# Performance work log

Hardware: AMD Instinct MI355X
Metric: run time of the kernel (lower is better)

## Reference

```python
import jax, jax.numpy as jnp
import numpy as np

N, G, HID, LAT, E_RAND = 20000, 3000, 256, 32, 320000
EPS = 1e-8
NEG_SLOPE = 0.2  # PyG GATv2Conv default leaky_relu slope


def _segment_softmax(logits, seg, n):
    # numerically stable softmax over edges grouped by destination node
    m = jax.ops.segment_max(logits, seg, num_segments=n)
    ex = jnp.exp(logits - m[seg])
    s = jax.ops.segment_sum(ex, seg, num_segments=n)
    return ex / (s[seg] + 1e-16)


def _gatv2(x, src, dst, Wl, Wr, att, b, n):
    # GATv2 (heads=1): score = att . leaky_relu(Wl x_j + Wr x_i)
    xl = x @ Wl  # [N, C] source transform (also the message)
    xr = x @ Wr  # [N, C] destination transform
    e = jax.nn.leaky_relu(xl[src] + xr[dst], NEG_SLOPE)  # [E, C]
    logit = e @ att  # [E]
    alpha = _segment_softmax(logit, dst, n)
    out = jax.ops.segment_sum(alpha[:, None] * xl[src], dst, num_segments=n)
    return out + b


def _log_zinb(x, mu, theta, pi):
    theta = theta[None, :]
    softplus_pi = jax.nn.softplus(-pi)
    log_theta_eps = jnp.log(theta + EPS)
    log_theta_mu_eps = jnp.log(theta + mu + EPS)
    pi_theta_log = -pi + theta * (log_theta_eps - log_theta_mu_eps)
    case_zero = jax.nn.softplus(pi_theta_log) - softplus_pi
    case_nz = (-softplus_pi + pi_theta_log
               + x * (jnp.log(mu + EPS) - log_theta_mu_eps)
               + jax.lax.lgamma(x + theta) - jax.lax.lgamma(theta)
               - jax.lax.lgamma(x + 1.0))
    return jnp.where(x < EPS, case_zero, 0.0) + jnp.where(x > EPS, case_nz, 0.0)


def setup_inputs():
    key = jax.random.key(0)
    ks = jax.random.split(key, 14)
    x = jax.random.randint(ks[0], (N, G), 0, 20).astype(jnp.float32)
    er = jax.random.randint(ks[1], (2, E_RAND), 0, N, dtype=jnp.int32)
    loops = jnp.tile(jnp.arange(N, dtype=jnp.int32)[None, :], (2, 1))
    edge_index = jnp.concatenate([er, loops], axis=1)  # [2, 340000] incl self-loops
    noise = jax.random.normal(ks[2], (N, LAT), dtype=jnp.float32)

    def init(k, shape, fan_in):
        return jax.random.normal(k, shape, dtype=jnp.float32) / np.float32(np.sqrt(fan_in))

    Wl1 = init(ks[3], (G, HID), G); Wr1 = init(ks[4], (G, HID), G)
    att1 = init(ks[5], (HID,), HID); b1 = jnp.zeros((HID,), jnp.float32)
    Wl2 = init(ks[6], (HID, 2 * LAT), HID); Wr2 = init(ks[7], (HID, 2 * LAT), HID)
    att2 = init(ks[8], (2 * LAT,), 2 * LAT); b2 = jnp.zeros((2 * LAT,), jnp.float32)
    Wd1 = init(ks[9], (LAT, HID), LAT); bd1 = jnp.zeros((HID,), jnp.float32)
    Wd2 = init(ks[10], (HID, G), HID); bd2 = jnp.zeros((G,), jnp.float32)
    Wdo = init(ks[11], (HID, G), HID); bdo = jnp.zeros((G,), jnp.float32)
    theta = jax.random.uniform(ks[12], (G,), minval=0.5, maxval=2.0, dtype=jnp.float32)
    return dict(x=x, edge_index=edge_index, noise=noise,
                Wl1=Wl1, Wr1=Wr1, att1=att1, b1=b1,
                Wl2=Wl2, Wr2=Wr2, att2=att2, b2=b2,
                Wd1=Wd1, bd1=bd1, Wd2=Wd2, bd2=bd2, Wdo=Wdo, bdo=bdo,
                theta=theta)


def reference(x, edge_index, noise, Wl1, Wr1, att1, b1, Wl2, Wr2, att2, b2,
              Wd1, bd1, Wd2, bd2, Wdo, bdo, theta):
    n = x.shape[0]
    src, dst = edge_index[0], edge_index[1]
    # --- GATv2 encoder ---
    h = _gatv2(x, src, dst, Wl1, Wr1, att1, b1, n)
    h2 = _gatv2(jax.nn.relu(h), src, dst, Wl2, Wr2, att2, b2, n)  # [N, 2*LAT]
    mu_z, logvar = h2[:, :LAT], h2[:, LAT:]
    # --- reparameterize: std = sqrt(exp(logvar)) ---
    z = mu_z + noise * jnp.exp(0.5 * logvar)
    # --- ZINB decoder ---
    hd = z @ Wd1 + bd1
    mean = jax.nn.softplus(hd @ Wd2 + bd2)
    pi = hd @ Wdo + bdo
    # --- loss: -E[log ZINB] + KL(q(z|x) || N(0,I)) ---
    recon = -jnp.mean(jnp.sum(_log_zinb(x, mean, theta, pi), axis=1))
    kl = jnp.mean(0.5 * jnp.sum(mu_z ** 2 + jnp.exp(logvar) - logvar - 1.0, axis=1))
    return recon + kl
```

## Files before the change

### kernel.cpp

```cpp
#include <hip/hip_runtime.h>
#include <math.h>

#define NN   20000
#define GG   3000
#define HIDD 256
#define LATT 32
#define KP1  3008
#define FEPS 1e-8f

typedef __attribute__((ext_vector_type(8))) __bf16 bf16x8;
typedef __attribute__((ext_vector_type(4))) float f32x4;

__device__ __forceinline__ float fsp(float v) {
    float t = __expf(-fabsf(v));
    return fmaxf(v, 0.f) + __logf(1.f + t);
}
__device__ __forceinline__ float sp_approx(float t) {
    float a = fabsf(t);
    float den = fmaf(a, fmaf(a, fmaf(a, 0.8382f, -1.4958f), 1.87f), 1.f);
    return fmaxf(t, 0.f) + 0.6931472f * __builtin_amdgcn_rcpf(den);
}
__device__ __forceinline__ float lrelu(float v) {
    return v > 0.f ? v : 0.2f * v;
}
__device__ __forceinline__ ushort f2bf(float f) {
    uint b = __float_as_uint(f);
    return (ushort)((b + 0x7FFFu + ((b >> 16) & 1u)) >> 16);
}
__device__ __forceinline__ float bf2f(ushort u) {
    return __uint_as_float((uint)u << 16);
}
__device__ __forceinline__ uint pk2(float a, float b) {
    return (uint)f2bf(a) | ((uint)f2bf(b) << 16);
}
__device__ __forceinline__ void gload16(const void* g, void* l) {
    __builtin_amdgcn_global_load_lds((const __attribute__((address_space(1))) void*)g,
                                     (__attribute__((address_space(3))) void*)l, 16, 0, 0);
}

__global__ __launch_bounds__(256)
void x2bf(const float* __restrict__ x, ushort* __restrict__ xb) {
    const int CH = KP1 / 8;
    size_t i = (size_t)blockIdx.x * 256 + threadIdx.x;
    if (i >= (size_t)NN * CH) return;
    size_t row = i / CH;
    int c8 = (int)(i % CH) * 8;
    uint4 w = make_uint4(0u, 0u, 0u, 0u);
    if (c8 < GG) {
        const float* p = x + row * GG + c8;
        float4 a = ((const float4*)p)[0];
        float4 b = ((const float4*)p)[1];
        w.x = pk2(a.x, a.y); w.y = pk2(a.z, a.w);
        w.z = pk2(b.x, b.y); w.w = pk2(b.z, b.w);
    }
    *(uint4*)(xb + row * KP1 + c8) = w;
}

__global__ void zinb_table(const float* __restrict__ theta, float* __restrict__ tabL,
                           float* __restrict__ logte, int G_) {
    int idx = blockIdx.x * blockDim.x + threadIdx.x;
    if (idx >= G_ * 20) return;
    int g = idx / 20, c = idx % 20;
    float th = theta[g];
    tabL[idx] = lgammaf((float)c + th) - lgammaf(th) - lgammaf((float)c + 1.f);
    if (c == 0) logte[g] = logf(th + FEPS);
}

__global__ void edge_hist(const int* __restrict__ ei, int* __restrict__ cnt, int E) {
    int e = blockIdx.x * blockDim.x + threadIdx.x;
    if (e < E) atomicAdd(&cnt[ei[E + e]], 1);
}

__global__ __launch_bounds__(1024)
void scan_deg(int* __restrict__ cnt_cur, int* __restrict__ rowptr, int Nn) {
    __shared__ int ts[1024];
    int t = threadIdx.x;
    int chunk = (Nn + 1023) / 1024;
    int beg = t * chunk, end = min(beg + chunk, Nn);
    int s = 0;
    for (int i = beg; i < end; i++) s += cnt_cur[i];
    ts[t] = s;
    __syncthreads();
    for (int off = 1; off < 1024; off <<= 1) {
        int v = (t >= off) ? ts[t - off] : 0;
        __syncthreads();
        ts[t] += v;
        __syncthreads();
    }
    int run = (t == 0) ? 0 : ts[t - 1];
    for (int i = beg; i < end; i++) {
        int c = cnt_cur[i];
        rowptr[i] = run;
        cnt_cur[i] = run;
        run += c;
    }
    if (t == 1023) rowptr[Nn] = ts[1023];
}

__global__ void edge_scatter(const int* __restrict__ ei, int* __restrict__ cur,
                             int* __restrict__ eidx, int E) {
    int e = blockIdx.x * blockDim.x + threadIdx.x;
    if (e < E) {
        int p = atomicAdd(&cur[ei[E + e]], 1);
        eidx[p] = e;
    }
}

__global__ __launch_bounds__(256)
void transp_bf16(const float* __restrict__ in, ushort* __restrict__ out,
                 int K, int N, int Kpad) {
    __shared__ ushort t[32][33];
    int k0 = blockIdx.x * 32, n0 = blockIdx.y * 32;
    int tx = threadIdx.x & 31, ty = threadIdx.x >> 5;
    #pragma unroll
    for (int u = 0; u < 32; u += 8) {
        int k = k0 + ty + u, n = n0 + tx;
        t[ty + u][tx] = (k < K && n < N) ? f2bf(in[(size_t)k * N + n]) : (ushort)0;
    }
    __syncthreads();
    #pragma unroll
    for (int u = 0; u < 32; u += 8) {
        int n = n0 + ty + u, k = k0 + tx;
        if (n < N && k < Kpad) out[(size_t)n * Kpad + k] = t[tx][ty + u];
    }
}

__global__ __launch_bounds__(256)
void wcomb(const float* __restrict__ Wd1, const float* __restrict__ bd1,
           const float* __restrict__ Wd2, const float* __restrict__ bd2,
           const float* __restrict__ Wdo, const float* __restrict__ bdo,
           ushort* __restrict__ W2t, ushort* __restrict__ Wot,
           float* __restrict__ b2c, float* __restrict__ boc, int G_) {
    __shared__ float w1s[32 * 256];
    int tid = threadIdx.x;
    for (int i = tid; i < 32 * 256; i += 256) w1s[i] = Wd1[i];
    __syncthreads();
    int gl = tid & 63, rg = tid >> 6;
    int g = blockIdx.x * 64 + gl;
    int gc = min(g, G_ - 1);
    float a2[8], ao[8];
    #pragma unroll
    for (int i = 0; i < 8; i++) { a2[i] = 0.f; ao[i] = 0.f; }
    float ab2 = 0.f, abo = 0.f;
    for (int j = 0; j < 256; j++) {
        float w2 = Wd2[(size_t)j * G_ + gc];
        float wo = Wdo[(size_t)j * G_ + gc];
        if (rg == 0) {
            float b1 = bd1[j];
            ab2 = fmaf(b1, w2, ab2);
            abo = fmaf(b1, wo, abo);
        }
        #pragma unroll
        for (int i = 0; i < 8; i++) {
            float w1 = w1s[(rg * 8 + i) * 256 + j];
            a2[i] = fmaf(w1, w2, a2[i]);
            ao[i] = fmaf(w1, wo, ao[i]);
        }
    }
    if (g < G_) {
        #pragma unroll
        for (int i = 0; i < 8; i++) {
            W2t[(size_t)g * 32 + rg * 8 + i] = f2bf(a2[i]);
            Wot[(size_t)g * 32 + rg * 8 + i] = f2bf(ao[i]);
        }
        if (rg == 0) { b2c[g] = ab2 + bd2[g]; boc[g] = abo + bdo[g]; }
    }
}

__global__ __launch_bounds__(256, 8)
void dec_zinb(const ushort* __restrict__ zb, const ushort* __restrict__ W2t,
              const ushort* __restrict__ Wot, const ushort* __restrict__ xb,
              const float* __restrict__ tabL, const float* __restrict__ theta,
              const float* __restrict__ logte, const float* __restrict__ b2c,
              const float* __restrict__ boc, double* __restrict__ partsR,
              int M, int G_) {
    __shared__ __align__(16) char xs[16384];
    __shared__ float tabs[64 * 20];
    __shared__ float thetas[64], thltes[64], bd2s[64], bdos[64];
    __shared__ double redd[4];
    const int tid = threadIdx.x;
    const int nwg = gridDim.x * gridDim.y;
    const int orig = blockIdx.y * gridDim.x + blockIdx.x;
    const int q = nwg >> 3, r = nwg & 7, xcd = orig & 7;
    const int vv = (xcd < r ? xcd * (q + 1) : r * (q + 1) + (xcd - r) * q) + (orig >> 3);
    const int bx = vv % gridDim.x, by = vv / gridDim.x;
    const int m0 = by * 128, n0 = bx * 64;
    const int lane = tid & 63, wid = tid >> 6;
    const int wr = wid >> 1, wc = wid & 1;
    const int frow = lane & 15;
    const int ksl = (lane >> 4) << 3;

    {
        const int row_in8 = lane >> 3;
        const int ch = lane & 7;
        #pragma unroll
        for (int u = 0; u < 4; u++) {
            int s = (wid << 2) + u;
            int rr = (s << 3) + row_in8;
            int gm = m0 + rr; if (gm > M - 1) gm = M - 1;
            int csw = ch ^ (rr & 7);
            size_t go = (size_t)gm * KP1 + n0 + (csw << 3);
            gload16(xb + go, xs + (s << 10) + (lane << 4));
        }
    }

    for (int i = tid; i < 64; i += 256) {
        int g = n0 + i;
        bool ok = g < G_;
        float th = ok ? theta[g] : 1.f;
        thetas[i] = th;
        thltes[i] = ok ? th * logte[g] : 0.f;
        bd2s[i]   = ok ? b2c[g] : 0.f;
        bdos[i]   = ok ? boc[g] : 0.f;
    }
    for (int i = tid; i < 64 * 20; i += 256) {
        int g = n0 + i / 20;
        tabs[i] = (g < G_) ? tabL[(size_t)g * 20 + i % 20] : 0.f;
    }

    f32x4 acc1[4][2], acc2[4][2];
    #pragma unroll
    for (int i = 0; i < 4; i++)
        #pragma unroll
        for (int j = 0; j < 2; j++) {
            acc1[i][j] = (f32x4){0.f, 0.f, 0.f, 0.f};
            acc2[i][j] = (f32x4){0.f, 0.f, 0.f, 0.f};
        }

    bf16x8 af[4];
    #pragma unroll
    for (int mi = 0; mi < 4; mi++) {
        int gm = min(m0 + (wr << 6) + (mi << 4) + frow, M - 1);
        af[mi] = *(const bf16x8*)(zb + (size_t)gm * 32 + ksl);
    }
    #pragma unroll
    for (int ni = 0; ni < 2; ni++) {
        int gn = min(n0 + (wc << 5) + (ni << 4) + frow, G_ - 1);
        bf16x8 bf1 = *(const bf16x8*)(W2t + (size_t)gn * 32 + ksl);
        bf16x8 bf2 = *(const bf16x8*)(Wot + (size_t)gn * 32 + ksl);
        #pragma unroll
        for (int mi = 0; mi < 4; mi++) {
            acc1[mi][ni] = __builtin_amdgcn_mfma_f32_16x16x32_bf16(af[mi], bf1, acc1[mi][ni], 0, 0, 0);
            acc2[mi][ni] = __builtin_amdgcn_mfma_f32_16x16x32_bf16(af[mi], bf2, acc2[mi][ni], 0, 0, 0);
        }
    }
    __syncthreads();

    const int lr = (lane >> 4) << 2;
    float lsum = 0.f;
    #pragma unroll
    for (int mi = 0; mi < 4; mi++)
        #pragma unroll
        for (int ni = 0; ni < 2; ni++) {
            int lcol = (wc << 5) + (ni << 4) + frow;
            int gn = n0 + lcol;
            int lrow0 = (wr << 6) + (mi << 4) + lr;
            if (gn >= G_) continue;
            f32x4 am = acc1[mi][ni], ap = acc2[mi][ni];
            float th = thetas[lcol], thlte = thltes[lcol];
            float bm = bd2s[lcol], bp = bdos[lcol];
            #pragma unroll
            for (int j = 0; j < 4; j++) {
                int lrow = lrow0 + j;
                if (m0 + lrow >= M) continue;
                int o = (lrow << 7) + ((((lcol >> 3) ^ (lrow & 7)) << 4)) + ((lcol & 7) << 1);
                float xv = bf2f(*(const ushort*)(xs + o));
                float mu  = fsp(am[j] + bm);
                float pi  = ap[j] + bp;
                float spp = fsp(pi);
                float ltme = __logf(th + mu + FEPS);
                float lmu  = __logf(mu + FEPS);
                int xi = (int)(xv + 0.5f);
                float ptl = fmaf(-th, ltme, thlte) - pi;
                float corr = (xv < FEPS) ? sp_approx(-ptl) : 0.f;
                lsum += thlte + tabs[lcol * 20 + xi] - spp
                      - (th + xv) * ltme + xv * lmu + corr;
            }
        }
    #pragma unroll
    for (int off = 32; off; off >>= 1) lsum += __shfl_down(lsum, off);
    if (lane == 0) redd[wid] = (double)lsum;
    __syncthreads();
    if (tid == 0)
        partsR[by * gridDim.x + bx] = redd[0] + redd[1] + redd[2] + redd[3];
}

__global__ __launch_bounds__(512, 4)
void gemm_big(const ushort* __restrict__ At, const ushort* __restrict__ B1t,
              const ushort* __restrict__ B2t, ushort* __restrict__ C1,
              ushort* __restrict__ C2, int M, int Kpad, int Nc) {
    __shared__ __align__(16) char lds[49152];
    char* ldsA  = lds;
    char* ldsB1 = lds + 16384;
    char* ldsB2 = lds + 32768;

    const int tid = threadIdx.x;
    const int nwg = gridDim.x * gridDim.y;
    const int orig = blockIdx.y * gridDim.x + blockIdx.x;
    const int q = nwg >> 3, r = nwg & 7, xcd = orig & 7;
    const int vv = (xcd < r ? xcd * (q + 1) : r * (q + 1) + (xcd - r) * q) + (orig >> 3);
    const int bx = vv % gridDim.x, by = vv / gridDim.x;
    const int m0 = by * 128, n0 = bx * 128;
    const int lane = tid & 63, wid = tid >> 6;
    const int wr = wid >> 2, wc = wid & 3;
    const int frow = lane & 15;
    const int fkb = (lane >> 4) << 4;

    const int row_in = lane >> 3;
    const int sch = (lane & 7) ^ (row_in & 7);
    const int ldso = (lane << 4);

    f32x4 acc1[4][2], acc2[4][2];
    #pragma unroll
    for (int i = 0; i < 4; i++)
        #pragma unroll
        for (int j = 0; j < 2; j++) {
            acc1[i][j] = (f32x4){0.f, 0.f, 0.f, 0.f};
            acc2[i][j] = (f32x4){0.f, 0.f, 0.f, 0.f};
        }

    const int nk = Kpad >> 6;
    for (int t = 0; t < nk; t++) {
        const int k0 = t << 6;
        #pragma unroll
        for (int u = 0; u < 2; u++) {
            int s = (wid << 1) + u;
            int gnb = n0 + (s << 3) + row_in;
            size_t gob = (size_t)gnb * Kpad + k0 + (sch << 3);
            gload16(B1t + gob, ldsB1 + (s << 10) + ldso);
            gload16(B2t + gob, ldsB2 + (s << 10) + ldso);
            int gma = m0 + (s << 3) + row_in;
            if (gma > M - 1) gma = M - 1;
            size_t goa = (size_t)gma * Kpad + k0 + (sch << 3);
            gload16(At + goa, ldsA + (s << 10) + ldso);
        }
        __syncthreads();
        #pragma unroll
        for (int kk = 0; kk < 2; kk++) {
            int kb = (kk << 6) + fkb;
            bf16x8 af[4], b1f[2], b2f[2];
            #pragma unroll
            for (int mi = 0; mi < 4; mi++) {
                int rr = (wr << 6) + (mi << 4) + frow;
                int o = ((rr << 7) + kb) ^ ((rr & 7) << 4);
                af[mi] = *(const bf16x8*)(ldsA + o);
            }
            #pragma unroll
            for (int ni = 0; ni < 2; ni++) {
                int rr = (wc << 5) + (ni << 4) + frow;
                int o = ((rr << 7) + kb) ^ ((rr & 7) << 4);
                b1f[ni] = *(const bf16x8*)(ldsB1 + o);
                b2f[ni] = *(const bf16x8*)(ldsB2 + o);
            }
            #pragma unroll
            for (int mi = 0; mi < 4; mi++)
                #pragma unroll
                for (int ni = 0; ni < 2; ni++) {
                    acc1[mi][ni] = __builtin_amdgcn_mfma_f32_16x16x32_bf16(af[mi], b1f[ni], acc1[mi][ni], 0, 0, 0);
                    acc2[mi][ni] = __builtin_amdgcn_mfma_f32_16x16x32_bf16(af[mi], b2f[ni], acc2[mi][ni], 0, 0, 0);
                }
        }
        __syncthreads();
    }

    const int lr = (lane >> 4) << 2;
    #pragma unroll
    for (int mi = 0; mi < 4; mi++)
        #pragma unroll
        for (int ni = 0; ni < 2; ni++) {
            int gmb = m0 + (wr << 6) + (mi << 4) + lr;
            int gn  = n0 + (wc << 5) + (ni << 4) + frow;
            if (gn >= Nc) continue;
            f32x4 v1 = acc1[mi][ni], v2 = acc2[mi][ni];
            #pragma unroll
            for (int j = 0; j < 4; j++) {
                int gm = gmb + j;
                if (gm < M) {
                    C1[(size_t)gm * Nc + gn] = f2bf(v1[j]);
                    C2[(size_t)gm * Nc + gn] = f2bf(v2[j]);
                }
            }
        }
}

__global__ __launch_bounds__(256, 4)
void mfma_dual(const void* __restrict__ Ap, const ushort* __restrict__ B1t,
               const ushort* __restrict__ B2t, float* __restrict__ C1,
               float* __restrict__ C2, int M, int K, int Nc) {
    __shared__ __align__(16) char lds[24576];
    char* ldsA  = lds;
    char* ldsB1 = lds + 8192;
    char* ldsB2 = lds + 16384;

    const int tid = threadIdx.x;
    const int m0 = blockIdx.y * 64, n0 = blockIdx.x * 64;
    const int lane = tid & 63, wid = tid >> 6;
    const int wr = wid >> 1, wc = wid & 1;
    const int frow = lane & 15;
    const int fkb = (lane >> 4) << 4;

    f32x4 acc1[2][2], acc2[2][2];
    #pragma unroll
    for (int i = 0; i < 2; i++)
        #pragma unroll
        for (int j = 0; j < 2; j++) {
            acc1[i][j] = (f32x4){0.f, 0.f, 0.f, 0.f};
            acc2[i][j] = (f32x4){0.f, 0.f, 0.f, 0.f};
        }

    const int nk = (K + 63) >> 6;
    for (int t = 0; t < nk; t++) {
        const int k0 = t << 6;
        #pragma unroll
        for (int u = 0; u < 2; u++) {
            int c = tid + (u << 8);
            int row = c >> 3, col8 = (c & 7) << 3;
            int gm = m0 + row, gk = k0 + col8;
            uint4 w = make_uint4(0u, 0u, 0u, 0u);
            if (gm < M && gk < K)
                w = *(const uint4*)((const ushort*)Ap + (size_t)gm * K + gk);
            int o = ((row << 7) + (col8 << 1)) ^ ((row & 7) << 4);
            *(uint4*)(ldsA + o) = w;
        }
        #pragma unroll
        for (int u = 0; u < 2; u++) {
            int c = tid + (u << 8);
            int row = c >> 3, col8 = (c & 7) << 3;
            int gn = n0 + row, gk = k0 + col8;
            uint4 w1 = make_uint4(0u, 0u, 0u, 0u), w2 = w1;
            if (gn < Nc && gk < K) {
                size_t o = (size_t)gn * K + gk;
                w1 = *(const uint4*)(B1t + o);
                w2 = *(const uint4*)(B2t + o);
            }
            int o = ((row << 7) + (col8 << 1)) ^ ((row & 7) << 4);
            *(uint4*)(ldsB1 + o) = w1;
            *(uint4*)(ldsB2 + o) = w2;
        }
        __syncthreads();
        #pragma unroll
        for (int kk = 0; kk < 2; kk++) {
            int kb = (kk << 6) + fkb;
            bf16x8 af[2], b1f[2], b2f[2];
            #pragma unroll
            for (int mi = 0; mi < 2; mi++) {
                int rr = (wr << 5) + (mi << 4) + frow;
                int o = ((rr << 7) + kb) ^ ((rr & 7) << 4);
                af[mi] = *(const bf16x8*)(ldsA + o);
            }
            #pragma unroll
            for (int ni = 0; ni < 2; ni++) {
                int rr = (wc << 5) + (ni << 4) + frow;
                int o = ((rr << 7) + kb) ^ ((rr & 7) << 4);
                b1f[ni] = *(const bf16x8*)(ldsB1 + o);
                b2f[ni] = *(const bf16x8*)(ldsB2 + o);
            }
            #pragma unroll
            for (int mi = 0; mi < 2; mi++)
                #pragma unroll
                for (int ni = 0; ni < 2; ni++) {
                    acc1[mi][ni] = __builtin_amdgcn_mfma_f32_16x16x32_bf16(af[mi], b1f[ni], acc1[mi][ni], 0, 0, 0);
                    acc2[mi][ni] = __builtin_amdgcn_mfma_f32_16x16x32_bf16(af[mi], b2f[ni], acc2[mi][ni], 0, 0, 0);
                }
        }
        __syncthreads();
    }

    const int lr = (lane >> 4) << 2;
    #pragma unroll
    for (int mi = 0; mi < 2; mi++)
        #pragma unroll
        for (int ni = 0; ni < 2; ni++) {
            int gmb = m0 + (wr << 5) + (mi << 4) + lr;
            int gn  = n0 + (wc << 5) + (ni << 4) + frow;
            if (gn >= Nc) continue;
            f32x4 v1 = acc1[mi][ni], v2 = acc2[mi][ni];
            #pragma unroll
            for (int j = 0; j < 4; j++) {
                int gm = gmb + j;
                if (gm < M) {
                    C1[(size_t)gm * Nc + gn] = v1[j];
                    C2[(size_t)gm * Nc + gn] = v2[j];
                }
            }
        }
}

template<int DW, int OM, int IBF>
__global__ __launch_bounds__(256)
void gat_attn(const void* __restrict__ xlv, const void* __restrict__ xrv,
              const float* __restrict__ att, const int* __restrict__ ei,
              const int* __restrict__ rowptr, const int* __restrict__ eidx,
              const float* __restrict__ bias, void* __restrict__ out,
              int D, int Nn) {
    int wid = threadIdx.x >> 6, lane = threadIdx.x & 63;
    int n = blockIdx.x * 4 + wid;
    if (n >= Nn) return;
    int k = lane * DW;
    float xrr[DW], ats[DW], hacc[DW];
    if (DW == 4) {
        float4 a4 = *(const float4*)(att + k);
        ats[0] = a4.x; ats[1] = a4.y; ats[2] = a4.z; ats[3] = a4.w;
        if (IBF) {
            ushort4 u = *(const ushort4*)((const ushort*)xrv + (size_t)n * D + k);
            xrr[0] = bf2f(u.x); xrr[1] = bf2f(u.y); xrr[2] = bf2f(u.z); xrr[3] = bf2f(u.w);
        } else {
            float4 r4 = *(const float4*)((const float*)xrv + (size_t)n * D + k);
            xrr[0] = r4.x; xrr[1] = r4.y; xrr[2] = r4.z; xrr[3] = r4.w;
        }
    } else {
        ats[0] = att[k];
        xrr[0] = IBF ? bf2f(((const ushort*)xrv)[(size_t)n * D + k])
                     : ((const float*)xrv)[(size_t)n * D + k];
    }
    #pragma unroll
    for (int d = 0; d < DW; d++) hacc[d] = 0.f;
    float m = -3.0e38f, ssum = 0.f;
    int beg = rowptr[n], end = rowptr[n + 1];
    for (int j = beg; j < end; j++) {
        int e = eidx[j];
        int src = ei[e];
        float v[DW];
        float p;
        if (DW == 4) {
            if (IBF) {
                ushort4 u = *(const ushort4*)((const ushort*)xlv + (size_t)src * D + k);
                v[0] = bf2f(u.x); v[1] = bf2f(u.y); v[2] = bf2f(u.z); v[3] = bf2f(u.w);
            } else {
                float4 v4 = *(const float4*)((const float*)xlv + (size_t)src * D + k);
                v[0] = v4.x; v[1] = v4.y; v[2] = v4.z; v[3] = v4.w;
            }
            p = ats[0] * lrelu(v[0] + xrr[0]) + ats[1] * lrelu(v[1] + xrr[1])
              + ats[2] * lrelu(v[2] + xrr[2]) + ats[3] * lrelu(v[3] + xrr[3]);
        } else {
            v[0] = IBF ? bf2f(((const ushort*)xlv)[(size_t)src * D + k])
                       : ((const float*)xlv)[(size_t)src * D + k];
            p = ats[0] * lrelu(v[0] + xrr[0]);
        }
        #pragma unroll
        for (int o2 = 32; o2; o2 >>= 1) p += __shfl_xor(p, o2);
        float mnew = fmaxf(m, p);
        float sc = __expf(m - mnew);
        float w  = __expf(p - mnew);
        ssum = fmaf(ssum, sc, w);
        #pragma unroll
        for (int d = 0; d < DW; d++) hacc[d] = fmaf(hacc[d], sc, w * v[d]);
        m = mnew;
    }
    float inv = 1.f / (ssum + 1e-16f);
    if (DW == 4) {
        float4 b = *(const float4*)(bias + k);
        float r0 = fmaf(hacc[0], inv, b.x), r1 = fmaf(hacc[1], inv, b.y);
        float r2 = fmaf(hacc[2], inv, b.z), r3 = fmaf(hacc[3], inv, b.w);
        if (OM == 0) {
            *(float4*)((float*)out + (size_t)n * D + k) = make_float4(r0, r1, r2, r3);
        } else {
            ushort4 o;
            o.x = f2bf(fmaxf(r0, 0.f)); o.y = f2bf(fmaxf(r1, 0.f));
            o.z = f2bf(fmaxf(r2, 0.f)); o.w = f2bf(fmaxf(r3, 0.f));
            *(ushort4*)((ushort*)out + (size_t)n * D + k) = o;
        }
    } else {
        float r0 = fmaf(hacc[0], inv, bias[k]);
        if (OM == 0) ((float*)out)[(size_t)n * D + k] = r0;
        else         ((ushort*)out)[(size_t)n * D + k] = f2bf(fmaxf(r0, 0.f));
    }
}

__global__ __launch_bounds__(256)
void z_kl(const float* __restrict__ h2, const float* __restrict__ noise,
          ushort* __restrict__ z, double* __restrict__ partsK, int Nn) {
    __shared__ double rd[4];
    int gid = blockIdx.x * blockDim.x + threadIdx.x;
    int n = gid >> 5, k = gid & 31;
    float kt = 0.f;
    if (n < Nn) {
        float mu = h2[(size_t)n * 64 + k];
        float lv = h2[(size_t)n * 64 + 32 + k];
        float ev = expf(lv);
        z[(size_t)n * 32 + k] = f2bf(mu + noise[(size_t)n * 32 + k] * expf(0.5f * lv));
        kt = 0.5f * (mu * mu + ev - lv - 1.f);
    }
    #pragma unroll
    for (int off = 32; off; off >>= 1) kt += __shfl_down(kt, off);
    int wid = threadIdx.x >> 6, lane = threadIdx.x & 63;
    if (lane == 0) rd[wid] = (double)kt;
    __syncthreads();
    if (threadIdx.x == 0) partsK[blockIdx.x] = rd[0] + rd[1] + rd[2] + rd[3];
}

__global__ __launch_bounds__(256)
void final_reduce(const double* __restrict__ pR, int nR,
                  const double* __restrict__ pK, int nK,
                  float* __restrict__ out, int Nn) {
    __shared__ double sd[256];
    double s = 0.0;
    for (int i = threadIdx.x; i < nR; i += 256) s -= pR[i];
    for (int i = threadIdx.x; i < nK; i += 256) s += pK[i];
    sd[threadIdx.x] = s;
    __syncthreads();
    for (int o = 128; o; o >>= 1) {
        if (threadIdx.x < o) sd[threadIdx.x] += sd[threadIdx.x + o];
        __syncthreads();
    }
    if (threadIdx.x == 0) out[0] = (float)(sd[0] / (double)Nn);
}

extern "C" void kernel_launch(void* const* d_in, const int* in_sizes, int n_in,
                              void* d_out, int out_size, void* d_ws, size_t ws_size,
                              hipStream_t stream) {
    const int N_ = NN, G_ = GG, HID_ = HIDD;
    const float* x     = (const float*)d_in[0];
    const int*   ei    = (const int*)d_in[1];
    const float* noise = (const float*)d_in[2];
    const float* Wl1   = (const float*)d_in[3];
    const float* Wr1   = (const float*)d_in[4];
    const float* att1  = (const float*)d_in[5];
    const float* b1    = (const float*)d_in[6];
    const float* Wl2   = (const float*)d_in[7];
    const float* Wr2   = (const float*)d_in[8];
    const float* att2  = (const float*)d_in[9];
    const float* b2    = (const float*)d_in[10];
    const float* Wd1   = (const float*)d_in[11];
    const float* bd1   = (const float*)d_in[12];
    const float* Wd2   = (const float*)d_in[13];
    const float* bd2   = (const float*)d_in[14];
    const float* Wdo   = (const float*)d_in[15];
    const float* bdo   = (const float*)d_in[16];
    const float* theta = (const float*)d_in[17];
    const int E = in_sizes[1] / 2;

    const int MB128 = (N_ + 127) / 128;
    const int DGX   = (G_ + 63) / 64;
    const int nR    = DGX * MB128;
    const int nKb   = (N_ * 32) / 256;

    char* base = (char*)d_ws;
    size_t off = 0;
    auto alloc = [&](size_t bytes) -> char* {
        char* p = base + off;
        off = (off + bytes + 255) & ~(size_t)255;
        return p;
    };
    double* partsR = (double*)alloc((size_t)nR * 8);
    double* partsK = (double*)alloc((size_t)nKb * 8);
    float*  tabL  = (float*)alloc((size_t)G_ * 20 * 4);
    float*  logte = (float*)alloc((size_t)G_ * 4);
    int*    rowptr= (int*)alloc((size_t)(N_ + 1) * 4);
    int*    cur   = (int*)alloc((size_t)N_ * 4);
    int*    eidx  = (int*)alloc((size_t)E * 4);
    ushort* Wl1t  = (ushort*)alloc((size_t)HID_ * KP1 * 2);
    ushort* Wr1t  = (ushort*)alloc((size_t)HID_ * KP1 * 2);
    ushort* Wl2t  = (ushort*)alloc((size_t)64 * HID_ * 2);
    ushort* Wr2t  = (ushort*)alloc((size_t)64 * HID_ * 2);
    ushort* W2t   = (ushort*)alloc((size_t)G_ * 32 * 2);
    ushort* Wot   = (ushort*)alloc((size_t)G_ * 32 * 2);
    float*  b2c   = (float*)alloc((size_t)G_ * 4);
    float*  boc   = (float*)alloc((size_t)G_ * 4);
    ushort* xb    = (ushort*)alloc((size_t)N_ * KP1 * 2);
    ushort* xl1b  = (ushort*)alloc((size_t)N_ * HID_ * 2);
    ushort* xr1b  = (ushort*)alloc((size_t)N_ * HID_ * 2);
    ushort* h_bf  = (ushort*)alloc((size_t)N_ * HID_ * 2);
    float*  xl2 = (float*)xl1b;
    float*  xr2 = xl2 + (size_t)N_ * 64;
    float*  h2  = xr2 + (size_t)N_ * 64;
    ushort* zb  = (ushort*)(h2 + (size_t)N_ * 64);

    float*  outf = (float*)d_out;

    hipMemsetAsync(cur, 0, N_ * sizeof(int), stream);

    x2bf<<<(int)(((size_t)N_ * (KP1 / 8) + 255) / 256), 256, 0, stream>>>(x, xb);
    zinb_table<<<(G_ * 20 + 255) / 256, 256, 0, stream>>>(theta, tabL, logte, G_);
    edge_hist<<<(E + 255) / 256, 256, 0, stream>>>(ei, cur, E);
    scan_deg<<<1, 1024, 0, stream>>>(cur, rowptr, N_);
    edge_scatter<<<(E + 255) / 256, 256, 0, stream>>>(ei, cur, eidx, E);

    transp_bf16<<<dim3(KP1 / 32, (HID_ + 31) / 32), 256, 0, stream>>>(Wl1, Wl1t, G_, HID_, KP1);
    transp_bf16<<<dim3(KP1 / 32, (HID_ + 31) / 32), 256, 0, stream>>>(Wr1, Wr1t, G_, HID_, KP1);
    transp_bf16<<<dim3(HID_ / 32, 2), 256, 0, stream>>>(Wl2, Wl2t, HID_, 64, HID_);
    transp_bf16<<<dim3(HID_ / 32, 2), 256, 0, stream>>>(Wr2, Wr2t, HID_, 64, HID_);

    wcomb<<<(G_ + 63) / 64, 256, 0, stream>>>(
        Wd1, bd1, Wd2, bd2, Wdo, bdo, W2t, Wot, b2c, boc, G_);

    gemm_big<<<dim3(HID_ / 128, MB128), 512, 0, stream>>>(
        xb, Wl1t, Wr1t, xl1b, xr1b, N_, KP1, HID_);
    gat_attn<4, 1, 1><<<(N_ + 3) / 4, 256, 0, stream>>>(
        xl1b, xr1b, att1, ei, rowptr, eidx, b1, h_bf, HID_, N_);

    mfma_dual<<<dim3(1, (N_ + 63) / 64), 256, 0, stream>>>(
        h_bf, Wl2t, Wr2t, xl2, xr2, N_, HID_, 64);
    gat_attn<1, 0, 0><<<(N_ + 3) / 4, 256, 0, stream>>>(
        xl2, xr2, att2, ei, rowptr, eidx, b2, h2, 64, N_);

    z_kl<<<nKb, 256, 0, stream>>>(h2, noise, zb, partsK, N_);

    dec_zinb<<<dim3(DGX, MB128), 256, 0, stream>>>(
        zb, W2t, Wot, xb, tabL, theta, logte, b2c, boc, partsR, N_, G_);

    final_reduce<<<1, 256, 0, stream>>>(partsR, nR, partsK, nKb, outf, N_);
}
```

Baseline: 644.3 us.

## Transpose decoder MFMA so genes map to rows and read x directly from global

The ZINB decoder kernel now computes the transposed product: weights are the A operand with 128 genes per tile and z is the B operand with 64 cells per tile. Each lane now owns four consecutive genes for one cell, so it reads x straight from global as a 4-element vector and picks up per-gene parameters with float4 LDS loads. This removes the swizzled LDS staging of the x tile. The theta*log(theta) term is folded into the lgamma table, and the occupancy hint drops from 8 to 4 waves per SIMD. The cost is narrow, strided 8-byte global loads of x in place of the coalesced 16-byte async tile loads.

```diff
diff --git a/kernel.cpp b/kernel.cpp
--- a/kernel.cpp
+++ b/kernel.cpp
@@ -167,16 +167,15 @@
     }
 }
 
-__global__ __launch_bounds__(256, 8)
+__global__ __launch_bounds__(256, 4)
 void dec_zinb(const ushort* __restrict__ zb, const ushort* __restrict__ W2t,
               const ushort* __restrict__ Wot, const ushort* __restrict__ xb,
               const float* __restrict__ tabL, const float* __restrict__ theta,
               const float* __restrict__ logte, const float* __restrict__ b2c,
               const float* __restrict__ boc, double* __restrict__ partsR,
               int M, int G_) {
-    __shared__ __align__(16) char xs[16384];
-    __shared__ float tabs[64 * 20];
-    __shared__ float thetas[64], thltes[64], bd2s[64], bdos[64];
+    __shared__ float tabs[128 * 20];
+    __shared__ float thetas[128], thltes[128], bd2s[128], bdos[128];
     __shared__ double redd[4];
     const int tid = threadIdx.x;
     const int nwg = gridDim.x * gridDim.y;
@@ -184,28 +183,14 @@
     const int q = nwg >> 3, r = nwg & 7, xcd = orig & 7;
     const int vv = (xcd < r ? xcd * (q + 1) : r * (q + 1) + (xcd - r) * q) + (orig >> 3);
     const int bx = vv % gridDim.x, by = vv / gridDim.x;
-    const int m0 = by * 128, n0 = bx * 64;
+    const int g0 = bx * 128, n0 = by * 64;
     const int lane = tid & 63, wid = tid >> 6;
     const int wr = wid >> 1, wc = wid & 1;
     const int frow = lane & 15;
     const int ksl = (lane >> 4) << 3;
 
-    {
-        const int row_in8 = lane >> 3;
-        const int ch = lane & 7;
-        #pragma unroll
-        for (int u = 0; u < 4; u++) {
-            int s = (wid << 2) + u;
-            int rr = (s << 3) + row_in8;
-            int gm = m0 + rr; if (gm > M - 1) gm = M - 1;
-            int csw = ch ^ (rr & 7);
-            size_t go = (size_t)gm * KP1 + n0 + (csw << 3);
-            gload16(xb + go, xs + (s << 10) + (lane << 4));
-        }
-    }
-
-    for (int i = tid; i < 64; i += 256) {
-        int g = n0 + i;
+    for (int i = tid; i < 128; i += 256) {
+        int g = g0 + i;
         bool ok = g < G_;
         float th = ok ? theta[g] : 1.f;
         thetas[i] = th;
@@ -213,9 +198,9 @@
         bd2s[i]   = ok ? b2c[g] : 0.f;
         bdos[i]   = ok ? boc[g] : 0.f;
     }
-    for (int i = tid; i < 64 * 20; i += 256) {
-        int g = n0 + i / 20;
-        tabs[i] = (g < G_) ? tabL[(size_t)g * 20 + i % 20] : 0.f;
+    for (int i = tid; i < 128 * 20; i += 256) {
+        int gl = i / 20, g = g0 + gl;
+        tabs[i] = (g < G_) ? (tabL[(size_t)g * 20 + i % 20] + theta[g] * logte[g]) : 0.f;
     }
 
     f32x4 acc1[4][2], acc2[4][2];
@@ -227,56 +212,66 @@
             acc2[i][j] = (f32x4){0.f, 0.f, 0.f, 0.f};
         }
 
-    bf16x8 af[4];
+    bf16x8 a2f[4], aof[4], bzf[2];
     #pragma unroll
     for (int mi = 0; mi < 4; mi++) {
-        int gm = min(m0 + (wr << 6) + (mi << 4) + frow, M - 1);
-        af[mi] = *(const bf16x8*)(zb + (size_t)gm * 32 + ksl);
+        int gg = min(g0 + (wr << 6) + (mi << 4) + frow, G_ - 1);
+        a2f[mi] = *(const bf16x8*)(W2t + (size_t)gg * 32 + ksl);
+        aof[mi] = *(const bf16x8*)(Wot + (size_t)gg * 32 + ksl);
     }
     #pragma unroll
     for (int ni = 0; ni < 2; ni++) {
-        int gn = min(n0 + (wc << 5) + (ni << 4) + frow, G_ - 1);
-        bf16x8 bf1 = *(const bf16x8*)(W2t + (size_t)gn * 32 + ksl);
-        bf16x8 bf2 = *(const bf16x8*)(Wot + (size_t)gn * 32 + ksl);
-        #pragma unroll
-        for (int mi = 0; mi < 4; mi++) {
-            acc1[mi][ni] = __builtin_amdgcn_mfma_f32_16x16x32_bf16(af[mi], bf1, acc1[mi][ni], 0, 0, 0);
-            acc2[mi][ni] = __builtin_amdgcn_mfma_f32_16x16x32_bf16(af[mi], bf2, acc2[mi][ni], 0, 0, 0);
-        }
-    }
+        int nn = min(n0 + (wc << 5) + (ni << 4) + frow, M - 1);
+        bzf[ni] = *(const bf16x8*)(zb + (size_t)nn * 32 + ksl);
+    }
+    #pragma unroll
+    for (int mi = 0; mi < 4; mi++)
+        #pragma unroll
+        for (int ni = 0; ni < 2; ni++) {
+            acc1[mi][ni] = __builtin_amdgcn_mfma_f32_16x16x32_bf16(a2f[mi], bzf[ni], acc1[mi][ni], 0, 0, 0);
+            acc2[mi][ni] = __builtin_amdgcn_mfma_f32_16x16x32_bf16(aof[mi], bzf[ni], acc2[mi][ni], 0, 0, 0);
+        }
     __syncthreads();
 
     const int lr = (lane >> 4) << 2;
     float lsum = 0.f;
     #pragma unroll
-    for (int mi = 0; mi < 4; mi++)
+    for (int mi = 0; mi < 4; mi++) {
+        int gl0 = (wr << 6) + (mi << 4) + lr;
+        int gj0 = g0 + gl0;
+        if (gj0 >= G_) continue;
+        float4 th4 = *(const float4*)&thetas[gl0];
+        float4 b24 = *(const float4*)&bd2s[gl0];
+        float4 bo4 = *(const float4*)&bdos[gl0];
+        float4 tl4 = *(const float4*)&thltes[gl0];
+        float ths[4] = {th4.x, th4.y, th4.z, th4.w};
+        float b2s[4] = {b24.x, b24.y, b24.z, b24.w};
+        float bos[4] = {bo4.x, bo4.y, bo4.z, bo4.w};
+        float tls[4] = {tl4.x, tl4.y, tl4.z, tl4.w};
         #pragma unroll
         for (int ni = 0; ni < 2; ni++) {
-            int lcol = (wc << 5) + (ni << 4) + frow;
-            int gn = n0 + lcol;
-            int lrow0 = (wr << 6) + (mi << 4) + lr;
-            if (gn >= G_) continue;
+            int nn = n0 + (wc << 5) + (ni << 4) + frow;
+            if (nn >= M) continue;
+            ushort4 xu = *(const ushort4*)(xb + (size_t)nn * KP1 + gj0);
+            float xvs[4] = {bf2f(xu.x), bf2f(xu.y), bf2f(xu.z), bf2f(xu.w)};
             f32x4 am = acc1[mi][ni], ap = acc2[mi][ni];
-            float th = thetas[lcol], thlte = thltes[lcol];
-            float bm = bd2s[lcol], bp = bdos[lcol];
             #pragma unroll
             for (int j = 0; j < 4; j++) {
-                int lrow = lrow0 + j;
-                if (m0 + lrow >= M) continue;
-                int o = (lrow << 7) + ((((lcol >> 3) ^ (lrow & 7)) << 4)) + ((lcol & 7) << 1);
-                float xv = bf2f(*(const ushort*)(xs + o));
-                float mu  = fsp(am[j] + bm);
-                float pi  = ap[j] + bp;
+                float th = ths[j];
+                float mu  = fsp(am[j] + b2s[j]);
+                float pi  = ap[j] + bos[j];
                 float spp = fsp(pi);
                 float ltme = __logf(th + mu + FEPS);
                 float lmu  = __logf(mu + FEPS);
+                float xv = xvs[j];
                 int xi = (int)(xv + 0.5f);
-                float ptl = fmaf(-th, ltme, thlte) - pi;
+                float ptl = fmaf(-th, ltme, tls[j]) - pi;
                 float corr = (xv < FEPS) ? sp_approx(-ptl) : 0.f;
-                lsum += thlte + tabs[lcol * 20 + xi] - spp
-                      - (th + xv) * ltme + xv * lmu + corr;
-            }
-        }
+                float base = tabs[(gl0 + j) * 20 + xi] - spp + corr;
+                lsum += fmaf(xv, lmu - ltme, fmaf(-th, ltme, base));
+            }
+        }
+    }
     #pragma unroll
     for (int off = 32; off; off >>= 1) lsum += __shfl_down(lsum, off);
     if (lane == 0) redd[wid] = (double)lsum;
@@ -631,8 +626,9 @@
     const int E = in_sizes[1] / 2;
 
     const int MB128 = (N_ + 127) / 128;
-    const int DGX   = (G_ + 63) / 64;
-    const int nR    = DGX * MB128;
+    const int DGB   = (G_ + 127) / 128;
+    const int DNB   = (N_ + 63) / 64;
+    const int nR    = DGB * DNB;
     const int nKb   = (N_ * 32) / 256;
 
     char* base = (char*)d_ws;
@@ -696,7 +692,7 @@
 
     z_kl<<<nKb, 256, 0, stream>>>(h2, noise, zb, partsK, N_);
 
-    dec_zinb<<<dim3(DGX, MB128), 256, 0, stream>>>(
+    dec_zinb<<<dim3(DGB, DNB), 256, 0, stream>>>(
         zb, W2t, Wot, xb, tabL, theta, logte, b2c, boc, partsR, N_, G_);
 
     final_reduce<<<1, 256, 0, stream>>>(partsR, nR, partsK, nKb, outf, N_);
```

After: 631.9 us. About the same (-1.9%).
